# Kernel optimization log

Measured on AMD Instinct MI355X. Metric: run time of the kernel, lower is better.

The kernel has to match this reference:

```python
import jax, jax.numpy as jnp
import numpy as np

B, T, C, H = 32, 1024, 512, 1024
N_DATES, MAX_F = 64, 2048
SCALE = float(H) ** 0.5


def setup_inputs() -> dict:
    key = jax.random.key(0)
    k1, k2, k3, k4, k5, k6 = jax.random.split(key, 6)
    sd = 1.0 / C ** 0.5
    features = jax.random.normal(k1, (B, T, C), dtype=jnp.float32)
    features_timestamp = jax.random.randint(k2, (B, T), 0, MAX_F, dtype=jnp.int32)
    date_idx = jax.random.randint(k3, (B,), 0, N_DATES, dtype=jnp.int32)
    embed_spikes = jax.random.uniform(k4, (N_DATES, H, C), minval=-sd, maxval=sd, dtype=jnp.float32)
    embed_spikes_bias = jax.random.uniform(k5, (N_DATES,), minval=-sd, maxval=sd, dtype=jnp.float32)
    embed_pos = jax.random.normal(k6, (MAX_F, H), dtype=jnp.float32)
    return {
        "features": features,
        "features_timestamp": features_timestamp,
        "date_idx": date_idx,
        "embed_spikes": embed_spikes,
        "embed_spikes_bias": embed_spikes_bias,
        "embed_pos": embed_pos,
    }


def reference(features, features_timestamp, date_idx, embed_spikes, embed_spikes_bias, embed_pos):
    # gather per-sample weight [B, H, C], batched matmul -> [B, T, H]
    w = embed_spikes[date_idx]  # [B, H, C]
    x = jnp.einsum("bhc,btc->bth", w, features)
    x = x + embed_spikes_bias[date_idx][:, None, None]  # per-sample scalar bias
    x = x * SCALE
    x = x + embed_pos[features_timestamp]  # [B, T, H] positional add
    # dropout p=0.0 (eval) -> identity
    return x
```

## Files before the change

kernel.cpp:

```cpp
#include <hip/hip_runtime.h>
#include <hip/hip_bf16.h>
#include <stdint.h>

#define B_  32
#define T_  1024
#define C_  512
#define H_  1024
#define SCALE_ 32.0f

#define BM 128
#define BN 128
#define BK 32
#define ROWE 32
#define NSTEP (C_ / BK)

typedef __attribute__((ext_vector_type(8))) short frag_ab;
typedef __attribute__((ext_vector_type(4))) float frag_cd;

__device__ __forceinline__ unsigned short f2bf(float f) {
    union { float f; uint32_t u; } v; v.f = f;
    uint32_t u = v.u;
    return (unsigned short)((u + 0x7FFFu + ((u >> 16) & 1u)) >> 16);
}

__device__ __forceinline__ void cvt4_store(unsigned short* dst, float4 v) {
    union { unsigned short u[4]; uint2 d; } p;
    p.u[0] = f2bf(v.x); p.u[1] = f2bf(v.y); p.u[2] = f2bf(v.z); p.u[3] = f2bf(v.w);
    *(uint2*)dst = p.d;
}

__global__ __launch_bounds__(256, 4)
void NeuralEmbeddingLayer_kernel(
    const float* __restrict__ features,
    const int*   __restrict__ ts,
    const int*   __restrict__ date_idx,
    const float* __restrict__ spikes,
    const float* __restrict__ spikes_bias,
    const float* __restrict__ pos,
    float*       __restrict__ out)
{
    const int tid = threadIdx.x;
    const int bid = blockIdx.x;

    const int xcd   = bid & 7;
    const int local = bid >> 3;
    const int b     = ((local >> 6) << 3) + xcd;
    const int tile  = local & 63;
    const int ttile = tile >> 3;
    const int htile = tile & 7;
    const int t0 = ttile * BM;
    const int h0 = htile * BN;

    const int   date = date_idx[b];
    const float bias = spikes_bias[date];
    const float* A = features + ((size_t)b * T_ + t0) * C_;
    const float* W = spikes   + ((size_t)date * H_ + h0) * C_;

    __shared__ __align__(16) unsigned short ldsA[2][BM * ROWE];
    __shared__ __align__(16) unsigned short ldsB[2][BM * ROWE];
    __shared__ int lds_ts[BM];

    if (tid < BM) lds_ts[tid] = ts[b * T_ + t0 + tid];

    float4 pfA[4], pfB[4];

    auto gload = [&](const float* __restrict__ base, int i, int k0) -> float4 {
        int g = i * 256 + tid;
        int row = g >> 3, k4 = g & 7;
        return *(const float4*)(base + (size_t)row * C_ + k0 + k4 * 4);
    };
    auto stage = [&](int buf) {
#pragma unroll
        for (int i = 0; i < 4; ++i) {
            int g = i * 256 + tid;
            int row = g >> 3, j = g & 7;
            int s = (j >> 1) ^ ((row >> 1) & 3);
            int off = row * ROWE + s * 8 + (j & 1) * 4;
            cvt4_store(&ldsA[buf][off], pfA[i]);
            cvt4_store(&ldsB[buf][off], pfB[i]);
        }
    };

#pragma unroll
    for (int i = 0; i < 4; ++i) { pfA[i] = gload(A, i, 0); pfB[i] = gload(W, i, 0); }
    stage(0);
    __syncthreads();

    const int wave = tid >> 6;
    const int lane = tid & 63;
    const int quad = lane >> 4;
    const int m_   = lane & 15;
    const int wm = (wave >> 1) * 64;
    const int wn = (wave & 1) * 64;

    frag_cd acc[4][4] = {};

    for (int ks = 0; ks < NSTEP; ++ks) {
        const int buf = ks & 1;
        if (ks + 1 < NSTEP) {
            const int k0 = (ks + 1) * BK;
#pragma unroll
            for (int i = 0; i < 4; ++i) { pfA[i] = gload(A, i, k0); pfB[i] = gload(W, i, k0); }
        }

        frag_ab afrag[4], bfrag[4];
#pragma unroll
        for (int mi = 0; mi < 4; ++mi) {
            int row = wm + mi * 16 + m_;
            int sw  = (row >> 1) & 3;
            afrag[mi] = *(const frag_ab*)&ldsA[buf][row * ROWE + ((quad ^ sw) * 8)];
        }
#pragma unroll
        for (int ni = 0; ni < 4; ++ni) {
            int row = wn + ni * 16 + m_;
            int sw  = (row >> 1) & 3;
            bfrag[ni] = *(const frag_ab*)&ldsB[buf][row * ROWE + ((quad ^ sw) * 8)];
        }
#pragma unroll
        for (int mi = 0; mi < 4; ++mi)
#pragma unroll
            for (int ni = 0; ni < 4; ++ni)
                acc[mi][ni] = __builtin_amdgcn_mfma_f32_16x16x32_bf16(
                    afrag[mi], bfrag[ni], acc[mi][ni], 0, 0, 0);

        if (ks + 1 < NSTEP) stage((ks + 1) & 1);
        __syncthreads();
    }

#pragma unroll
    for (int mi = 0; mi < 4; ++mi) {
#pragma unroll
        for (int r = 0; r < 4; ++r) {
            int trow = wm + mi * 16 + quad * 4 + r;
            int tsv  = lds_ts[trow];
            const float* prow = pos + (size_t)tsv * H_ + h0;
            size_t orow = ((size_t)b * T_ + (t0 + trow)) * (size_t)H_ + h0;
#pragma unroll
            for (int ni = 0; ni < 4; ++ni) {
                int col = wn + ni * 16 + m_;
                out[orow + col] = acc[mi][ni][r] * SCALE_ + bias + prow[col];
            }
        }
    }
}

extern "C" void kernel_launch(void* const* d_in, const int* in_sizes, int n_in,
                              void* d_out, int out_size, void* d_ws, size_t ws_size,
                              hipStream_t stream) {
    const float* features  = (const float*)d_in[0];
    const int*   ts        = (const int*)d_in[1];
    const int*   date_idx  = (const int*)d_in[2];
    const float* spikes    = (const float*)d_in[3];
    const float* sbias     = (const float*)d_in[4];
    const float* pos       = (const float*)d_in[5];
    float*       out       = (float*)d_out;

    dim3 grid(B_ * (T_ / BM) * (H_ / BN));
    NeuralEmbeddingLayer_kernel<<<grid, 256, 0, stream>>>(
        features, ts, date_idx, spikes, sbias, pos, out);
}
```

Measured before the change: 316.5 us.

## Prefetch two K-steps ahead with hardware bf16 pack conversion

Deepens the global-to-register prefetch to two K-steps using two register sets, so each global load has a full iteration longer to land. The software bf16 rounding is replaced by the packed v_cvt_pk_bf16_f32 instruction, which cuts VALU work during staging. Other changes: a lighter custom barrier that waits only on LDS counters, a fully unrolled K loop, A fragments loaded per mi instead of all at once, and precomputed staging offsets. The extra prefetch registers raise register pressure, so launch bounds drop to 3 blocks per CU, which lowers occupancy.

```diff
diff --git a/kernel.cpp b/kernel.cpp
--- a/kernel.cpp
+++ b/kernel.cpp
@@ -1,5 +1,4 @@
 #include <hip/hip_runtime.h>
-#include <hip/hip_bf16.h>
 #include <stdint.h>
 
 #define B_  32
@@ -17,19 +16,26 @@
 typedef __attribute__((ext_vector_type(8))) short frag_ab;
 typedef __attribute__((ext_vector_type(4))) float frag_cd;
 
-__device__ __forceinline__ unsigned short f2bf(float f) {
-    union { float f; uint32_t u; } v; v.f = f;
-    uint32_t u = v.u;
-    return (unsigned short)((u + 0x7FFFu + ((u >> 16) & 1u)) >> 16);
+__device__ __forceinline__ uint32_t cvtpk_bf16(float lo, float hi) {
+    uint32_t r;
+    asm("v_cvt_pk_bf16_f32 %0, %1, %2" : "=v"(r) : "v"(lo), "v"(hi));
+    return r;
 }
 
 __device__ __forceinline__ void cvt4_store(unsigned short* dst, float4 v) {
-    union { unsigned short u[4]; uint2 d; } p;
-    p.u[0] = f2bf(v.x); p.u[1] = f2bf(v.y); p.u[2] = f2bf(v.z); p.u[3] = f2bf(v.w);
-    *(uint2*)dst = p.d;
+    uint2 p;
+    p.x = cvtpk_bf16(v.x, v.y);
+    p.y = cvtpk_bf16(v.z, v.w);
+    *(uint2*)dst = p;
 }
 
-__global__ __launch_bounds__(256, 4)
+#define BARRIER() do { \
+    asm volatile("s_waitcnt lgkmcnt(0)" ::: "memory"); \
+    __builtin_amdgcn_s_barrier(); \
+    asm volatile("" ::: "memory"); \
+} while (0)
+
+__global__ __launch_bounds__(256, 3)
 void NeuralEmbeddingLayer_kernel(
     const float* __restrict__ features,
     const int*   __restrict__ ts,
@@ -46,10 +52,8 @@
     const int local = bid >> 3;
     const int b     = ((local >> 6) << 3) + xcd;
     const int tile  = local & 63;
-    const int ttile = tile >> 3;
-    const int htile = tile & 7;
-    const int t0 = ttile * BM;
-    const int h0 = htile * BN;
+    const int t0 = (tile >> 3) * BM;
+    const int h0 = (tile & 7) * BN;
 
     const int   date = date_idx[b];
     const float bias = spikes_bias[date];
@@ -60,31 +64,36 @@
     __shared__ __align__(16) unsigned short ldsB[2][BM * ROWE];
     __shared__ int lds_ts[BM];
 
-    if (tid < BM) lds_ts[tid] = ts[b * T_ + t0 + tid];
+    const int r0  = tid >> 3;
+    const int c4  = (tid & 7) * 4;
+    const int jj  = tid & 7;
+    const int sw0 = (jj >> 1) ^ ((r0 >> 1) & 3);
+    const int offBase = r0 * ROWE + sw0 * 8 + (jj & 1) * 4;
 
-    float4 pfA[4], pfB[4];
+    float4 pA0[4], pB0[4], pA1[4], pB1[4];
 
-    auto gload = [&](const float* __restrict__ base, int i, int k0) -> float4 {
-        int g = i * 256 + tid;
-        int row = g >> 3, k4 = g & 7;
-        return *(const float4*)(base + (size_t)row * C_ + k0 + k4 * 4);
-    };
-    auto stage = [&](int buf) {
+    auto loadset = [&](float4 (&a)[4], float4 (&w)[4], int k0) {
 #pragma unroll
         for (int i = 0; i < 4; ++i) {
-            int g = i * 256 + tid;
-            int row = g >> 3, j = g & 7;
-            int s = (j >> 1) ^ ((row >> 1) & 3);
-            int off = row * ROWE + s * 8 + (j & 1) * 4;
-            cvt4_store(&ldsA[buf][off], pfA[i]);
-            cvt4_store(&ldsB[buf][off], pfB[i]);
+            a[i] = *(const float4*)(A + (size_t)(r0 + 32 * i) * C_ + (k0 + c4));
+            w[i] = *(const float4*)(W + (size_t)(r0 + 32 * i) * C_ + (k0 + c4));
+        }
+    };
+    auto stageset = [&](float4 (&a)[4], float4 (&w)[4], int buf) {
+#pragma unroll
+        for (int i = 0; i < 4; ++i) {
+            cvt4_store(&ldsA[buf][offBase + i * 1024], a[i]);
+            cvt4_store(&ldsB[buf][offBase + i * 1024], w[i]);
         }
     };
 
-#pragma unroll
-    for (int i = 0; i < 4; ++i) { pfA[i] = gload(A, i, 0); pfB[i] = gload(W, i, 0); }
-    stage(0);
-    __syncthreads();
+    int tsval = 0;
+    if (tid < BM) tsval = ts[b * T_ + t0 + tid];
+    loadset(pA0, pB0, 0);
+    loadset(pA1, pB1, BK);
+    if (tid < BM) lds_ts[tid] = tsval;
+    stageset(pA0, pB0, 0);
+    BARRIER();
 
     const int wave = tid >> 6;
     const int lane = tid & 63;
@@ -95,21 +104,16 @@
 
     frag_cd acc[4][4] = {};
 
+#pragma unroll
     for (int ks = 0; ks < NSTEP; ++ks) {
         const int buf = ks & 1;
-        if (ks + 1 < NSTEP) {
-            const int k0 = (ks + 1) * BK;
-#pragma unroll
-            for (int i = 0; i < 4; ++i) { pfA[i] = gload(A, i, k0); pfB[i] = gload(W, i, k0); }
+
+        if (ks + 2 < NSTEP) {
+            if ((ks & 1) == 0) loadset(pA0, pB0, (ks + 2) * BK);
+            else               loadset(pA1, pB1, (ks + 2) * BK);
         }
 
-        frag_ab afrag[4], bfrag[4];
-#pragma unroll
-        for (int mi = 0; mi < 4; ++mi) {
-            int row = wm + mi * 16 + m_;
-            int sw  = (row >> 1) & 3;
-            afrag[mi] = *(const frag_ab*)&ldsA[buf][row * ROWE + ((quad ^ sw) * 8)];
-        }
+        frag_ab bfrag[4];
 #pragma unroll
         for (int ni = 0; ni < 4; ++ni) {
             int row = wn + ni * 16 + m_;
@@ -117,14 +121,21 @@
             bfrag[ni] = *(const frag_ab*)&ldsB[buf][row * ROWE + ((quad ^ sw) * 8)];
         }
 #pragma unroll
-        for (int mi = 0; mi < 4; ++mi)
+        for (int mi = 0; mi < 4; ++mi) {
+            int row = wm + mi * 16 + m_;
+            int sw  = (row >> 1) & 3;
+            frag_ab af = *(const frag_ab*)&ldsA[buf][row * ROWE + ((quad ^ sw) * 8)];
 #pragma unroll
             for (int ni = 0; ni < 4; ++ni)
                 acc[mi][ni] = __builtin_amdgcn_mfma_f32_16x16x32_bf16(
-                    afrag[mi], bfrag[ni], acc[mi][ni], 0, 0, 0);
+                    af, bfrag[ni], acc[mi][ni], 0, 0, 0);
+        }
 
-        if (ks + 1 < NSTEP) stage((ks + 1) & 1);
-        __syncthreads();
+        if (ks + 1 < NSTEP) {
+            if ((ks & 1) == 0) stageset(pA1, pB1, buf ^ 1);
+            else               stageset(pA0, pB0, buf ^ 1);
+            BARRIER();
+        }
     }
 
 #pragma unroll
```

Result: slower. 327.7 us (+3.5%).
